# Kernel optimization log

Measured on AMD Instinct MI355X. Metric: run time of the kernel, lower is better.

## Reference

```python
import jax, jax.numpy as jnp
import numpy as np

B, T, D, H = 2, 2048, 2048, 16
HD = D // H


def setup_inputs() -> dict:
    key = jax.random.key(0)
    ks = jax.random.split(key, 6)
    s = 1.0 / np.sqrt(D)
    return {
        "x": jax.random.normal(ks[0], (B, T, D), dtype=jnp.float32),
        "Wq": jax.random.normal(ks[1], (D, D), dtype=jnp.float32) * s,
        "Wk": jax.random.normal(ks[2], (D, D), dtype=jnp.float32) * s,
        "Wv": jax.random.normal(ks[3], (D, D), dtype=jnp.float32) * s,
        "Wo": jax.random.normal(ks[4], (D, D), dtype=jnp.float32) * s,
        "bo": jnp.zeros((D,), dtype=jnp.float32),
    }


def reference(x, Wq, Wk, Wv, Wo, bo):
    b, t, d = x.shape
    # projections (torch Linear: x @ W.T)
    q = (x @ Wq.T).reshape(b, t, H, HD).transpose(0, 2, 1, 3)  # [B,H,T,HD]
    k = (x @ Wk.T).reshape(b, t, H, HD).transpose(0, 2, 1, 3)
    v = (x @ Wv.T).reshape(b, t, H, HD).transpose(0, 2, 1, 3)
    scores = jnp.einsum('bhid,bhjd->bhij', q, k) / np.sqrt(HD)  # [B,H,T,T]
    causal = jnp.tril(jnp.ones((t, t), dtype=bool))
    scores = jnp.where(causal[None, None], scores, -jnp.inf)
    attn = jax.nn.softmax(scores, axis=-1)
    out = jnp.einsum('bhij,bhjd->bhid', attn, v)  # [B,H,T,HD]
    out = out.transpose(0, 2, 1, 3).reshape(b, t, d)
    return out @ Wo.T + bo
```

## Files before the change

### kernel.cpp

```cpp
#include <hip/hip_runtime.h>
#include <hip/hip_bf16.h>

#define T_ 2048
#define D_ 2048
#define H_ 16
#define HD_ 128

typedef __hip_bfloat16 bf16;
using bf16x8 = __attribute__((ext_vector_type(8))) short;
using f32x4  = __attribute__((ext_vector_type(4))) float;

#define GLL16(g, l) __builtin_amdgcn_global_load_lds( \
    (const __attribute__((address_space(1))) void*)(g), \
    (__attribute__((address_space(3))) void*)(l), 16, 0, 0)

__device__ __forceinline__ f32x4 mfma16(bf16x8 a, bf16x8 b, f32x4 c) {
    return __builtin_amdgcn_mfma_f32_16x16x32_bf16(a, b, c, 0, 0, 0);
}

__global__ __launch_bounds__(256) void cast6(
    const float* __restrict__ s0, const float* __restrict__ s1,
    const float* __restrict__ s2, const float* __restrict__ s3,
    const float* __restrict__ s4, const float* __restrict__ s5,
    bf16* __restrict__ dst)
{
    int z = blockIdx.y;
    const float* s = (z == 0) ? s0 : (z == 1) ? s1 : (z == 2) ? s2
                   : (z == 3) ? s3 : (z == 4) ? s4 : s5;
    long i = ((long)blockIdx.x * 256 + threadIdx.x) * 8;
    float4 a = *(const float4*)(s + i);
    float4 b = *(const float4*)(s + i + 4);
    union { bf16 h[8]; int4 v; } u;
    u.h[0] = __float2bfloat16(a.x); u.h[1] = __float2bfloat16(a.y);
    u.h[2] = __float2bfloat16(a.z); u.h[3] = __float2bfloat16(a.w);
    u.h[4] = __float2bfloat16(b.x); u.h[5] = __float2bfloat16(b.y);
    u.h[6] = __float2bfloat16(b.z); u.h[7] = __float2bfloat16(b.w);
    *(int4*)(dst + (long)z * 4194304 + i) = u.v;
}


#define STAGE(t, b) do { \
    const bf16* Ag_ = Abase + (t)*32; \
    const bf16* Bg_ = Bbase + (t)*32; \
    GLL16(Ag_ + aoff0, As[b] + w*512); \
    GLL16(Ag_ + aoff1, As[b] + 2048 + w*512); \
    GLL16(Bg_ + aoff0, Bs[b] + w*512); \
    GLL16(Bg_ + aoff1, Bs[b] + 2048 + w*512); \
} while (0)

#define GEMM_MAINLOOP() \
    int tid = threadIdx.x, lane = tid & 63, w = tid >> 6; \
    int wm = w >> 1, wn = w & 1; \
    int srow = w*16 + (lane >> 2); \
     \
     \
    int scol = ((((lane & 3) - (srow >> 1)) & 3)) * 8; \
    long aoff0 = (long)srow * D_ + scol; \
    long aoff1 = aoff0 + 64L * D_; \
    f32x4 acc[4][4]; \
    _Pragma("unroll") \
    for (int i = 0; i < 4; ++i) \
        _Pragma("unroll") \
        for (int j = 0; j < 4; ++j) acc[i][j] = f32x4{0.f,0.f,0.f,0.f}; \
    STAGE(0, 0); STAGE(1, 1); STAGE(2, 2); \
    for (int kt = 0; kt < D_/32; ++kt) { \
        int rem = D_/32 - 1 - kt; \
        if (rem >= 2)      asm volatile("s_waitcnt vmcnt(8)" ::: "memory"); \
        else if (rem == 1) asm volatile("s_waitcnt vmcnt(4)" ::: "memory"); \
        else               asm volatile("s_waitcnt vmcnt(0)" ::: "memory"); \
        __builtin_amdgcn_s_barrier(); \
        asm volatile("" ::: "memory"); \
        int cb = kt & 3; \
        int g = lane >> 4; \
        bf16x8 af[4], bfr[4]; \
        _Pragma("unroll") \
        for (int mt = 0; mt < 4; ++mt) { \
            int r = wm*64 + mt*16 + (lane & 15); \
            af[mt] = *(const bf16x8*)&As[cb][r*32 + (((g + (r >> 1)) & 3) * 8)]; \
        } \
        _Pragma("unroll") \
        for (int nt = 0; nt < 4; ++nt) { \
            int r = wn*64 + nt*16 + (lane & 15); \
            bfr[nt] = *(const bf16x8*)&Bs[cb][r*32 + (((g + (r >> 1)) & 3) * 8)]; \
        } \
        if (kt + 3 < D_/32) { STAGE(kt + 3, (kt + 3) & 3); } \
        __builtin_amdgcn_s_setprio(1); \
        _Pragma("unroll") \
        for (int mt = 0; mt < 4; ++mt) \
            _Pragma("unroll") \
            for (int nt = 0; nt < 4; ++nt) \
                acc[mt][nt] = mfma16(af[mt], bfr[nt], acc[mt][nt]); \
        __builtin_amdgcn_s_setprio(0); \
    }

__global__ __launch_bounds__(256) void gemm_qkv(
    const bf16* __restrict__ xb,
    const bf16* __restrict__ wq, const bf16* __restrict__ wk, const bf16* __restrict__ wv,
    bf16* __restrict__ Qo, bf16* __restrict__ Ko, bf16* __restrict__ Vo)
{
    __shared__ bf16 As[4][128*32];
    __shared__ bf16 Bs[4][128*32];
    int z = blockIdx.z;
    const bf16* W = (z == 0) ? wq : (z == 1) ? wk : wv;
    bf16* out = (z == 0) ? Qo : (z == 1) ? Ko : Vo;
    int bn = blockIdx.x, bm = blockIdx.y;
    const bf16* Abase = xb + (long)bm * 128 * D_;
    const bf16* Bbase = W  + (long)bn * 128 * D_;

    GEMM_MAINLOOP();

    int mlo = bm*128 + wm*64;
    int nlo = bn*128 + wn*64;
    #pragma unroll
    for (int mt = 0; mt < 4; ++mt) {
        #pragma unroll
        for (int nt = 0; nt < 4; ++nt) {
            int n = nlo + nt*16 + (lane & 15);
            int h = n >> 7, hd = n & 127;
            #pragma unroll
            for (int r = 0; r < 4; ++r) {
                int m = mlo + mt*16 + (lane >> 4)*4 + r;
                int b = m >> 11, t = m & 2047;
                out[(((long)(b*H_ + h))*T_ + t)*HD_ + hd] = __float2bfloat16(acc[mt][nt][r]);
            }
        }
    }
}

__global__ __launch_bounds__(256) void attn(
    const bf16* __restrict__ Qm, const bf16* __restrict__ Km, const bf16* __restrict__ Vm,
    bf16* __restrict__ Om)
{
    __shared__ bf16 Ks[64*136];
    __shared__ bf16 Vt[128*72];
    __shared__ bf16 Ps[128*72];
    int bm = 15 - (blockIdx.x >> 5);
    int bh = blockIdx.x & 31;
    int tid = threadIdx.x, lane = tid & 63, w = tid >> 6;
    const float c1 = 0.12754012780914427f;
    const float c2 = 23.083120654223414f;
    const bf16* Qb = Qm + (long)bh*T_*HD_;
    const bf16* Kb = Km + (long)bh*T_*HD_;
    const bf16* Vb = Vm + (long)bh*T_*HD_;
    int m0 = bm*128 + w*32;

    bf16x8 qf[2][4];
    #pragma unroll
    for (int mt = 0; mt < 2; ++mt)
        #pragma unroll
        for (int ks = 0; ks < 4; ++ks)
            qf[mt][ks] = *(const bf16x8*)(Qb + (long)(m0 + mt*16 + (lane & 15))*HD_ + ks*32 + (lane >> 4)*8);

    bf16x8 onesB;
    {
        short v1 = ((lane & 15) == 0) ? (short)0x3F80 : (short)0;
        #pragma unroll
        for (int jj = 0; jj < 8; ++jj) onesB[jj] = v1;
    }

    f32x4 oacc[2][8];
    f32x4 lacc[2];
    #pragma unroll
    for (int mt = 0; mt < 2; ++mt) {
        lacc[mt] = f32x4{0.f,0.f,0.f,0.f};
        #pragma unroll
        for (int dt = 0; dt < 8; ++dt) oacc[mt][dt] = f32x4{0.f,0.f,0.f,0.f};
    }

    int krow = (tid >> 4);
    int kcg  = tid & 15;
    int njt = 2*bm + 2;

    bf16x8 kreg[4], vreg[4];
    #pragma unroll
    for (int i = 0; i < 4; ++i) {
        kreg[i] = *(const bf16x8*)(Kb + (long)(i*16 + krow)*HD_ + kcg*8);
        vreg[i] = *(const bf16x8*)(Vb + (long)lane*HD_ + (w + i*4)*8);
    }

    for (int j = 0; j < njt; ++j) {
        int j0 = j*64;
        __syncthreads();
        #pragma unroll
        for (int i = 0; i < 4; ++i)
            *(bf16x8*)&Ks[(i*16 + krow)*136 + kcg*8] = kreg[i];
        #pragma unroll
        for (int i = 0; i < 4; ++i) {
            int dg = w + i*4;
            union { bf16 h[8]; bf16x8 v; } u;
            u.v = vreg[i];
            #pragma unroll
            for (int jj = 0; jj < 8; ++jj)
                Vt[(dg*8 + jj)*72 + lane] = u.h[jj];
        }
        __syncthreads();

        if (j + 1 < njt) {
            int jn0 = j0 + 64;
            #pragma unroll
            for (int i = 0; i < 4; ++i) {
                kreg[i] = *(const bf16x8*)(Kb + (long)(jn0 + i*16 + krow)*HD_ + kcg*8);
                vreg[i] = *(const bf16x8*)(Vb + (long)(jn0 + lane)*HD_ + (w + i*4)*8);
            }
        }

        bool anyv  = (j0 <= m0 + 31);
        if (anyv) {
            bool bmask = (j0 + 63 > m0);
            f32x4 s[2][4];
            #pragma unroll
            for (int mt = 0; mt < 2; ++mt)
                #pragma unroll
                for (int nt = 0; nt < 4; ++nt) s[mt][nt] = f32x4{0.f,0.f,0.f,0.f};
            #pragma unroll
            for (int ks = 0; ks < 4; ++ks) {
                bf16x8 kf[4];
                #pragma unroll
                for (int nt = 0; nt < 4; ++nt)
                    kf[nt] = *(const bf16x8*)&Ks[(nt*16 + (lane & 15))*136 + ks*32 + (lane >> 4)*8];
                #pragma unroll
                for (int mt = 0; mt < 2; ++mt)
                    #pragma unroll
                    for (int nt = 0; nt < 4; ++nt)
                        s[mt][nt] = mfma16(qf[mt][ks], kf[nt], s[mt][nt]);
            }
            #pragma unroll
            for (int mt = 0; mt < 2; ++mt) {
                #pragma unroll
                for (int nt = 0; nt < 4; ++nt) {
                    int n = j0 + nt*16 + (lane & 15);
                    #pragma unroll
                    for (int r = 0; r < 4; ++r) {
                        float x = s[mt][nt][r] * c1 - c2;
                        if (bmask) {
                            int mg = m0 + mt*16 + (lane >> 4)*4 + r;
                            x = (n <= mg) ? x : -1e30f;
                        }
                        float p = exp2f(x);
                        int prow = w*32 + mt*16 + (lane >> 4)*4 + r;
                        Ps[prow*72 + nt*16 + (lane & 15)] = __float2bfloat16(p);
                    }
                }
            }
            #pragma unroll
            for (int kn = 0; kn < 2; ++kn) {
                bf16x8 pf[2], vf[8];
                #pragma unroll
                for (int mt = 0; mt < 2; ++mt)
                    pf[mt] = *(const bf16x8*)&Ps[(w*32 + mt*16 + (lane & 15))*72 + kn*32 + (lane >> 4)*8];
                #pragma unroll
                for (int dt = 0; dt < 8; ++dt)
                    vf[dt] = *(const bf16x8*)&Vt[(dt*16 + (lane & 15))*72 + kn*32 + (lane >> 4)*8];
                #pragma unroll
                for (int mt = 0; mt < 2; ++mt)
                    lacc[mt] = mfma16(pf[mt], onesB, lacc[mt]);
                #pragma unroll
                for (int mt = 0; mt < 2; ++mt)
                    #pragma unroll
                    for (int dt = 0; dt < 8; ++dt)
                        oacc[mt][dt] = mfma16(pf[mt], vf[dt], oacc[mt][dt]);
            }
        }
    }
    int b = bh >> 4, h = bh & 15;
    #pragma unroll
    for (int mt = 0; mt < 2; ++mt) {
        #pragma unroll
        for (int r = 0; r < 4; ++r) {
            float l = __shfl(lacc[mt][r], lane & 48, 64);
            float inv = 1.f / l;
            int t = m0 + mt*16 + (lane >> 4)*4 + r;
            #pragma unroll
            for (int dt = 0; dt < 8; ++dt) {
                int d = dt*16 + (lane & 15);
                Om[((long)(b*T_ + t))*D_ + h*HD_ + d] = __float2bfloat16(oacc[mt][dt][r] * inv);
            }
        }
    }
}

__global__ __launch_bounds__(256) void gemm_out(
    const bf16* __restrict__ Ab, const bf16* __restrict__ Wob,
    const float* __restrict__ bo, float* __restrict__ out)
{
    __shared__ bf16 As[4][128*32];
    __shared__ bf16 Bs[4][128*32];
    int bn = blockIdx.x, bm = blockIdx.y;
    const bf16* Abase = Ab  + (long)bm * 128 * D_;
    const bf16* Bbase = Wob + (long)bn * 128 * D_;

    GEMM_MAINLOOP();

    int mlo = bm*128 + wm*64;
    int nlo = bn*128 + wn*64;
    #pragma unroll
    for (int mt = 0; mt < 4; ++mt) {
        #pragma unroll
        for (int nt = 0; nt < 4; ++nt) {
            int n = nlo + nt*16 + (lane & 15);
            float bias = bo[n];
            #pragma unroll
            for (int r = 0; r < 4; ++r) {
                int m = mlo + mt*16 + (lane >> 4)*4 + r;
                out[(long)m*D_ + n] = acc[mt][nt][r] + bias;
            }
        }
    }
}

extern "C" void kernel_launch(void* const* d_in, const int* in_sizes, int n_in,
                              void* d_out, int out_size, void* d_ws, size_t ws_size,
                              hipStream_t stream) {
    const float* x  = (const float*)d_in[0];
    const float* Wq = (const float*)d_in[1];
    const float* Wk = (const float*)d_in[2];
    const float* Wv = (const float*)d_in[3];
    const float* Wo = (const float*)d_in[4];
    const float* bo = (const float*)d_in[5];
    float* out = (float*)d_out;

    bf16* ws  = (bf16*)d_ws;
    bf16* xb  = ws;
    bf16* wqb = ws + 8388608L;
    bf16* wkb = ws + 12582912L;
    bf16* wvb = ws + 16777216L;
    bf16* wob = ws + 20971520L;
    bf16* Qb  = ws + 25165824L;
    bf16* Kb  = ws + 33554432L;
    bf16* Vb  = ws + 41943040L;
    bf16* Ob  = xb;

    cast6<<<dim3(2048, 6), 256, 0, stream>>>(x, x + 4194304L, Wq, Wk, Wv, Wo, ws);
    gemm_qkv<<<dim3(16, 32, 3), 256, 0, stream>>>(xb, wqb, wkb, wvb, Qb, Kb, Vb);
    attn<<<512, 256, 0, stream>>>(Qb, Kb, Vb, Ob);
    gemm_out<<<dim3(16, 32), 256, 0, stream>>>(Ob, wob, bo, out);
}
```

Baseline: 390.7 us.

## Replace QKV GEMM with 256x256-tile 8-wave kernel over concatenated weights

```diff
diff --git a/kernel.cpp b/kernel.cpp
--- a/kernel.cpp
+++ b/kernel.cpp
@@ -39,6 +39,146 @@
 }
 
 
+#define SA(t, h, b) do { \
+    GLL16(Ab0 + (long)(h)*262144 + (t)*64,          &Asm[b][h][tid*8]); \
+    GLL16(Ab0 + (long)(h)*262144 + 131072 + (t)*64, &Asm[b][h][4096 + tid*8]); \
+} while (0)
+#define SB(t, h, b) do { \
+    GLL16(Bb0 + (long)(h)*262144 + (t)*64,          &Bsm[b][h][tid*8]); \
+    GLL16(Bb0 + (long)(h)*262144 + 131072 + (t)*64, &Bsm[b][h][4096 + tid*8]); \
+} while (0)
+
+#define RA(mf, ks) (*(const bf16x8*)&Asm[buf][wr][((mf)*16 + l15)*64 + ((((ks)*32) + g8) ^ swF)])
+#define RB(nf, ks) (*(const bf16x8*)&Bsm[buf][wc>>1][((wc&1)*64 + (nf)*16 + l15)*64 + ((((ks)*32) + g8) ^ swF)])
+
+#define PH_SYNC() do { \
+    __builtin_amdgcn_s_barrier(); \
+    asm volatile("s_waitcnt lgkmcnt(0)" ::: "memory"); \
+    __builtin_amdgcn_sched_barrier(0); \
+} while (0)
+
+__global__ __launch_bounds__(512) void gemm_qkv256(
+    const bf16* __restrict__ xb, const bf16* __restrict__ Wall,
+    bf16* __restrict__ QKV)
+{
+    __shared__ bf16 Asm[2][2][8192];
+    __shared__ bf16 Bsm[2][2][8192];
+    int tid = threadIdx.x, lane = tid & 63, wid = tid >> 6;
+    int wr = wid >> 2, wc = wid & 3;
+    int orig = blockIdx.x;
+    int wg = (orig & 7) * 48 + (orig >> 3);
+    int bm = wg / 24, bn = wg - bm * 24;
+
+    int sr  = tid >> 3;
+    int swS = ((sr >> 2) & 1) << 4;
+    int sc  = ((tid & 7) * 8) ^ swS;
+    const bf16* Ab0 = xb   + ((long)(bm * 256 + sr)) * 2048 + sc;
+    const bf16* Bb0 = Wall + ((long)(bn * 256 + sr)) * 2048 + sc;
+
+    int l15 = lane & 15, g8 = (lane >> 4) * 8;
+    int swF = ((lane >> 2) & 1) << 4;
+
+    f32x4 acc[8][4];
+    #pragma unroll
+    for (int i = 0; i < 8; ++i)
+        #pragma unroll
+        for (int j = 0; j < 4; ++j) acc[i][j] = f32x4{0.f, 0.f, 0.f, 0.f};
+
+    bf16x8 Ar[8][2];
+    bf16x8 Br[4][2];
+
+    SA(0, 0, 0); SA(0, 1, 0); SB(0, 0, 0); SB(0, 1, 0);
+    SA(1, 0, 1); SA(1, 1, 1);
+    asm volatile("s_waitcnt vmcnt(4)" ::: "memory");
+    __builtin_amdgcn_s_barrier();
+
+    const int NT = D_ / 64;
+    for (int t = 0; t < NT; ++t) {
+        int buf = t & 1, nbuf = buf ^ 1;
+        #pragma unroll
+        for (int mf = 0; mf < 4; ++mf) { Ar[mf][0] = RA(mf, 0); Ar[mf][1] = RA(mf, 1); }
+        #pragma unroll
+        for (int nf = 0; nf < 2; ++nf) { Br[nf][0] = RB(nf, 0); Br[nf][1] = RB(nf, 1); }
+        if (t + 1 < NT) SB(t + 1, 0, nbuf);
+        PH_SYNC();
+        __builtin_amdgcn_s_setprio(1);
+        #pragma unroll
+        for (int mf = 0; mf < 4; ++mf)
+            #pragma unroll
+            for (int nf = 0; nf < 2; ++nf) {
+                acc[mf][nf] = mfma16(Ar[mf][0], Br[nf][0], acc[mf][nf]);
+                acc[mf][nf] = mfma16(Ar[mf][1], Br[nf][1], acc[mf][nf]);
+            }
+        __builtin_amdgcn_s_setprio(0);
+        __builtin_amdgcn_s_barrier();
+        #pragma unroll
+        for (int mf = 4; mf < 8; ++mf) { Ar[mf][0] = RA(mf, 0); Ar[mf][1] = RA(mf, 1); }
+        if (t + 1 < NT) SB(t + 1, 1, nbuf);
+        PH_SYNC();
+        __builtin_amdgcn_s_setprio(1);
+        #pragma unroll
+        for (int mf = 4; mf < 8; ++mf)
+            #pragma unroll
+            for (int nf = 0; nf < 2; ++nf) {
+                acc[mf][nf] = mfma16(Ar[mf][0], Br[nf][0], acc[mf][nf]);
+                acc[mf][nf] = mfma16(Ar[mf][1], Br[nf][1], acc[mf][nf]);
+            }
+        __builtin_amdgcn_s_setprio(0);
+        __builtin_amdgcn_s_barrier();
+        #pragma unroll
+        for (int nf = 2; nf < 4; ++nf) { Br[nf][0] = RB(nf, 0); Br[nf][1] = RB(nf, 1); }
+        if (t + 2 < NT) SA(t + 2, 0, buf);
+        PH_SYNC();
+        __builtin_amdgcn_s_setprio(1);
+        #pragma unroll
+        for (int mf = 0; mf < 4; ++mf)
+            #pragma unroll
+            for (int nf = 2; nf < 4; ++nf) {
+                acc[mf][nf] = mfma16(Ar[mf][0], Br[nf][0], acc[mf][nf]);
+                acc[mf][nf] = mfma16(Ar[mf][1], Br[nf][1], acc[mf][nf]);
+            }
+        __builtin_amdgcn_s_setprio(0);
+        __builtin_amdgcn_s_barrier();
+        if (t + 2 < NT) {
+            SA(t + 2, 1, buf);
+            asm volatile("s_waitcnt vmcnt(4)" ::: "memory");
+        } else {
+            asm volatile("s_waitcnt vmcnt(0)" ::: "memory");
+        }
+        __builtin_amdgcn_s_barrier();
+        __builtin_amdgcn_s_setprio(1);
+        #pragma unroll
+        for (int mf = 4; mf < 8; ++mf)
+            #pragma unroll
+            for (int nf = 2; nf < 4; ++nf) {
+                acc[mf][nf] = mfma16(Ar[mf][0], Br[nf][0], acc[mf][nf]);
+                acc[mf][nf] = mfma16(Ar[mf][1], Br[nf][1], acc[mf][nf]);
+            }
+        __builtin_amdgcn_s_setprio(0);
+        __builtin_amdgcn_s_barrier();
+    }
+
+    int mBase = bm * 256 + wr * 128;
+    int nBase = bn * 256 + wc * 64;
+    #pragma unroll
+    for (int mf = 0; mf < 8; ++mf) {
+        #pragma unroll
+        for (int nf = 0; nf < 4; ++nf) {
+            int n = nBase + nf * 16 + l15;
+            int z = n >> 11, n2 = n & 2047;
+            int h = n2 >> 7, hd = n2 & 127;
+            #pragma unroll
+            for (int r = 0; r < 4; ++r) {
+                int m = mBase + mf * 16 + (lane >> 4) * 4 + r;
+                int b = m >> 11, tt = m & 2047;
+                QKV[(long)z * 8388608 + (((long)(b * H_ + h)) * T_ + tt) * HD_ + hd] =
+                    __float2bfloat16(acc[mf][nf][r]);
+            }
+        }
+    }
+}
+
+
 #define STAGE(t, b) do { \
     const bf16* Ag_ = Abase + (t)*32; \
     const bf16* Bg_ = Bbase + (t)*32; \
@@ -52,8 +192,6 @@
     int tid = threadIdx.x, lane = tid & 63, w = tid >> 6; \
     int wm = w >> 1, wn = w & 1; \
     int srow = w*16 + (lane >> 2); \
-     \
-     \
     int scol = ((((lane & 3) - (srow >> 1)) & 3)) * 8; \
     long aoff0 = (long)srow * D_ + scol; \
     long aoff1 = aoff0 + 64L * D_; \
@@ -93,40 +231,6 @@
         __builtin_amdgcn_s_setprio(0); \
     }
 
-__global__ __launch_bounds__(256) void gemm_qkv(
-    const bf16* __restrict__ xb,
-    const bf16* __restrict__ wq, const bf16* __restrict__ wk, const bf16* __restrict__ wv,
-    bf16* __restrict__ Qo, bf16* __restrict__ Ko, bf16* __restrict__ Vo)
-{
-    __shared__ bf16 As[4][128*32];
-    __shared__ bf16 Bs[4][128*32];
-    int z = blockIdx.z;
-    const bf16* W = (z == 0) ? wq : (z == 1) ? wk : wv;
-    bf16* out = (z == 0) ? Qo : (z == 1) ? Ko : Vo;
-    int bn = blockIdx.x, bm = blockIdx.y;
-    const bf16* Abase = xb + (long)bm * 128 * D_;
-    const bf16* Bbase = W  + (long)bn * 128 * D_;
-
-    GEMM_MAINLOOP();
-
-    int mlo = bm*128 + wm*64;
-    int nlo = bn*128 + wn*64;
-    #pragma unroll
-    for (int mt = 0; mt < 4; ++mt) {
-        #pragma unroll
-        for (int nt = 0; nt < 4; ++nt) {
-            int n = nlo + nt*16 + (lane & 15);
-            int h = n >> 7, hd = n & 127;
-            #pragma unroll
-            for (int r = 0; r < 4; ++r) {
-                int m = mlo + mt*16 + (lane >> 4)*4 + r;
-                int b = m >> 11, t = m & 2047;
-                out[(((long)(b*H_ + h))*T_ + t)*HD_ + hd] = __float2bfloat16(acc[mt][nt][r]);
-            }
-        }
-    }
-}
-
 __global__ __launch_bounds__(256) void attn(
     const bf16* __restrict__ Qm, const bf16* __restrict__ Km, const bf16* __restrict__ Vm,
     bf16* __restrict__ Om)
@@ -322,8 +426,6 @@
     bf16* ws  = (bf16*)d_ws;
     bf16* xb  = ws;
     bf16* wqb = ws + 8388608L;
-    bf16* wkb = ws + 12582912L;
-    bf16* wvb = ws + 16777216L;
     bf16* wob = ws + 20971520L;
     bf16* Qb  = ws + 25165824L;
     bf16* Kb  = ws + 33554432L;
@@ -331,7 +433,7 @@
     bf16* Ob  = xb;
 
     cast6<<<dim3(2048, 6), 256, 0, stream>>>(x, x + 4194304L, Wq, Wk, Wv, Wo, ws);
-    gemm_qkv<<<dim3(16, 32, 3), 256, 0, stream>>>(xb, wqb, wkb, wvb, Qb, Kb, Vb);
+    gemm_qkv256<<<dim3(384), 512, 0, stream>>>(xb, wqb, Qb);
     attn<<<512, 256, 0, stream>>>(Qb, Kb, Vb, Ob);
     gemm_out<<<dim3(16, 32), 256, 0, stream>>>(Ob, wob, bo, out);
 }
```

Result: slower. 415.0 us (+6.2%).
